# Performance work log

Hardware: AMD Instinct MI355X
Metric: run time of the kernel (lower is better)

The kernel has to match this reference:

```python
import jax, jax.numpy as jnp
import numpy as np

N_INST = 524288   # total instances across all bags
NF = 256          # feature dim
L = 128           # gated-attention hidden dim
C = 1             # num_classes
B = 4096          # num bags


def setup_inputs() -> dict:
    key = jax.random.key(0)
    k = jax.random.split(key, 6)
    # ragged bag sizes averaging ~128, deterministically summing to N_INST
    rng = np.random.RandomState(0)
    raw = rng.randint(64, 193, size=B).astype(np.int64)
    sizes = (raw * N_INST // raw.sum()).astype(np.int64)
    sizes[: int(N_INST - sizes.sum())] += 1  # distribute remainder (< B)
    assert sizes.sum() == N_INST
    s = 1.0 / np.sqrt(NF)
    return {
        "feats": jax.random.normal(k[0], (N_INST, NF), jnp.float32),
        "split_sizes": jnp.asarray(sizes, jnp.int64),
        "W_ins": jax.random.normal(k[1], (NF, C), jnp.float32) * s,
        "b_ins": jnp.zeros((C,), jnp.float32),
        "W_V": jax.random.normal(k[2], (NF, L), jnp.float32) * s,
        "b_V": jnp.zeros((L,), jnp.float32),
        "W_U": jax.random.normal(k[3], (NF, L), jnp.float32) * s,
        "b_U": jnp.zeros((L,), jnp.float32),
        "w_att": jax.random.normal(k[4], (L, 1), jnp.float32) * (1.0 / np.sqrt(L)),
        "b_att": jnp.zeros((1,), jnp.float32),
    }


def reference(feats, split_sizes, W_ins, b_ins, W_V, b_V, W_U, b_U, w_att, b_att):
    n = feats.shape[0]
    num_bags = split_sizes.shape[0]
    # segment id per instance (fused replacement of torch.split + Python loop)
    seg = jnp.repeat(jnp.arange(num_bags), split_sizes, total_repeat_length=n)

    # instance classifier (applied once to the whole ragged batch)
    inst_pred = feats @ W_ins + b_ins                      # [N, C]

    # gated attention scores
    gate = jnp.tanh(feats @ W_V + b_V) * jax.nn.sigmoid(feats @ W_U + b_U)
    scores = (gate @ w_att + b_att)[:, 0]                  # [N]

    # segmented softmax over each bag
    m = jax.ops.segment_max(scores, seg, num_segments=num_bags)  # [B]
    e = jnp.exp(scores - m[seg])
    denom = jax.ops.segment_sum(e, seg, num_segments=num_bags)   # [B]
    attn = e / denom[seg]                                        # [N]

    # bag prediction = attention-weighted sum of instance predictions
    bag_pred = jax.ops.segment_sum(attn[:, None] * inst_pred, seg,
                                   num_segments=num_bags)        # [B, C]
    return bag_pred, inst_pred
```

## Files before the change

### kernel.cpp

```cpp
#include <hip/hip_runtime.h>
#include <hip/hip_bf16.h>

#define N_INST 524288
#define NF     256
#define LDIM   128
#define NBAGS  4096
#define BM     64

typedef __attribute__((ext_vector_type(8)))  short          short8;
typedef __attribute__((ext_vector_type(16))) float          f32x16;
typedef __attribute__((ext_vector_type(4)))  unsigned short ushort4v;
typedef __attribute__((ext_vector_type(4)))  int            int4v;

__device__ __forceinline__ unsigned short f2bf(float f) {
    unsigned u = __float_as_uint(f);
    unsigned r = u + 0x7FFFu + ((u >> 16) & 1u);
    return (unsigned short)(r >> 16);
}

__global__ __launch_bounds__(256) void k_build(const float* __restrict__ W_V,
                                               const float* __restrict__ W_U,
                                               unsigned short* __restrict__ Bws) {
    int idx  = blockIdx.x * 256 + threadIdx.x;
    int j    = idx & 7;
    int lane = (idx >> 3) & 63;
    int ct   = (idx >> 9) & 7;
    int ks   = idx >> 12;
    int k    = ks * 16 + ((lane >> 5) << 3) + j;
    int n    = ((ct >> 1) << 5) + (lane & 31);
    const float* src = (ct & 1) ? W_U : W_V;
    Bws[idx] = f2bf(src[k * LDIM + n]);
}

__global__ __launch_bounds__(256) void k_scan(const int* __restrict__ sraw,
                                              int* __restrict__ offs) {
    __shared__ int csum[256];
    __shared__ int cpref[256];
    const int t = threadIdx.x;
    const bool is64 = (sraw[1] == 0);
    int local[16];
    int ssum = 0;
    for (int j = 0; j < 16; ++j) {
        int i = t * 16 + j;
        int v = is64 ? sraw[2 * i] : sraw[i];
        local[j] = v;
        ssum += v;
    }
    csum[t] = ssum;
    __syncthreads();
    if (t == 0) {
        int run = 0;
        for (int i = 0; i < 256; ++i) { cpref[i] = run; run += csum[i]; }
    }
    __syncthreads();
    int run = cpref[t];
    for (int j = 0; j < 16; ++j) { offs[t * 16 + j] = run; run += local[j]; }
    if (t == 255) offs[NBAGS] = run;
}

__global__ __launch_bounds__(256, 3) void k_gemm(
    const float* __restrict__ feats, const unsigned short* __restrict__ Bws,
    const float* __restrict__ W_ins, const float* __restrict__ b_ins,
    const float* __restrict__ b_V,   const float* __restrict__ b_U,
    const float* __restrict__ w_att, const float* __restrict__ b_att,
    float* __restrict__ scores, float* __restrict__ inst_out) {

    __shared__ unsigned short Al[2][1024];
    __shared__ float winsl[NF];
    __shared__ float bVl[LDIM], bUl[LDIM], wal[LDIM];
    __shared__ float Sp[BM][4];

    const int t    = threadIdx.x;
    const int lane = t & 63;
    const int cg   = t >> 6;
    const long r0  = (long)blockIdx.x * BM;

    const int row = t >> 2;
    const int q   = t & 3;

    winsl[t] = W_ins[t];
    if (t < LDIM) { bVl[t] = b_V[t]; bUl[t] = b_U[t]; wal[t] = w_att[t]; }

    const float*  arow = feats + (r0 + row) * NF + q * 4;
    const short8* bw   = (const short8*)Bws;

    const int aoff = ((row >> 5) * 64 + (q >> 1) * 32 + (row & 31)) * 8 + (q & 1) * 4;
    const int ctv  = cg * 2;
    const int ctu  = ctv + 1;

    float4 pa_0  = *(const float4*)(arow);
    short8 fbv_0 = bw[(0 * 8 + ctv) * 64 + lane];
    short8 fbu_0 = bw[(0 * 8 + ctu) * 64 + lane];
    float4 pa_1  = *(const float4*)(arow + 16);
    short8 fbv_1 = bw[(1 * 8 + ctv) * 64 + lane];
    short8 fbu_1 = bw[(1 * 8 + ctu) * 64 + lane];

    f32x16 accV0 = {}, accV1 = {};
    f32x16 accU0 = {}, accU1 = {};
    float pacc = 0.f;

    __syncthreads();

    #pragma unroll
    for (int ks = 0; ks < 16; ++ks) {
        const int X = ks & 1;
        float4 av  = X ? pa_1  : pa_0;
        short8 fbv = X ? fbv_1 : fbv_0;
        short8 fbu = X ? fbu_1 : fbu_0;

        float4 wv = *(const float4*)&winsl[ks * 16 + q * 4];
        pacc += av.x * wv.x + av.y * wv.y + av.z * wv.z + av.w * wv.w;

        ushort4v c;
        c.x = f2bf(av.x); c.y = f2bf(av.y); c.z = f2bf(av.z); c.w = f2bf(av.w);
        *(ushort4v*)&Al[X][aoff] = c;

        if (ks < 14) {
            if (X == 0) {
                pa_0  = *(const float4*)(arow + (ks + 2) * 16);
                fbv_0 = bw[((ks + 2) * 8 + ctv) * 64 + lane];
                fbu_0 = bw[((ks + 2) * 8 + ctu) * 64 + lane];
            } else {
                pa_1  = *(const float4*)(arow + (ks + 2) * 16);
                fbv_1 = bw[((ks + 2) * 8 + ctv) * 64 + lane];
                fbu_1 = bw[((ks + 2) * 8 + ctu) * 64 + lane];
            }
        }

        __syncthreads();

        short8 fa0 = *(const short8*)&Al[X][(0 * 64 + lane) * 8];
        short8 fa1 = *(const short8*)&Al[X][(1 * 64 + lane) * 8];
        accV0 = __builtin_amdgcn_mfma_f32_32x32x16_bf16(fa0, fbv, accV0, 0, 0, 0);
        accU0 = __builtin_amdgcn_mfma_f32_32x32x16_bf16(fa0, fbu, accU0, 0, 0, 0);
        accV1 = __builtin_amdgcn_mfma_f32_32x32x16_bf16(fa1, fbv, accV1, 0, 0, 0);
        accU1 = __builtin_amdgcn_mfma_f32_32x32x16_bf16(fa1, fbu, accU1, 0, 0, 0);
    }

    const int   c32 = lane & 31;
    const int   nn  = cg * 32 + c32;
    const float bv0s = bVl[nn], bu0s = bUl[nn], wn = wal[nn];
    const int   rh  = lane >> 5;

#define EPILOG(RT, AV, AU)                                                    \
    {                                                                         \
        _Pragma("unroll")                                                     \
        for (int r = 0; r < 16; ++r) {                                        \
            float v  = AV[r] + bv0s;                                          \
            float u  = AU[r] + bu0s;                                          \
            float ev = __expf(2.f * v);                                       \
            float th = 1.f - 2.f * __builtin_amdgcn_rcpf(ev + 1.f);           \
            float sg = __builtin_amdgcn_rcpf(1.f + __expf(-u));               \
            float x  = th * sg * wn;                                          \
            x += __shfl_xor(x, 1);                                            \
            x += __shfl_xor(x, 2);                                            \
            x += __shfl_xor(x, 4);                                            \
            x += __shfl_xor(x, 8);                                            \
            x += __shfl_xor(x, 16);                                           \
            if (c32 == 0)                                                     \
                Sp[RT * 32 + (r & 3) + 8 * (r >> 2) + 4 * rh][cg] = x;        \
        }                                                                     \
    }
    EPILOG(0, accV0, accU0)
    EPILOG(1, accV1, accU1)
#undef EPILOG

    float pt = pacc;
    pt += __shfl_xor(pt, 1);
    pt += __shfl_xor(pt, 2);
    if (q == 0) inst_out[r0 + row] = pt + b_ins[0];

    __syncthreads();
    if (t < BM)
        scores[r0 + t] = Sp[t][0] + Sp[t][1] + Sp[t][2] + Sp[t][3] + b_att[0];
}

__global__ __launch_bounds__(64) void k_bags(const int* __restrict__ offs,
                                             const float* __restrict__ scores,
                                             const float* __restrict__ inst,
                                             float* __restrict__ bag_out) {
    const int b    = blockIdx.x;
    const int lane = threadIdx.x;
    const int s0 = offs[b], s1 = offs[b + 1];
    float m = -1e30f;
    for (int i = s0 + lane; i < s1; i += 64) m = fmaxf(m, scores[i]);
    #pragma unroll
    for (int d = 32; d; d >>= 1) m = fmaxf(m, __shfl_xor(m, d));
    float se = 0.f, sp = 0.f;
    for (int i = s0 + lane; i < s1; i += 64) {
        float e = __expf(scores[i] - m);
        se += e;
        sp += e * inst[i];
    }
    #pragma unroll
    for (int d = 32; d; d >>= 1) { se += __shfl_xor(se, d); sp += __shfl_xor(sp, d); }
    if (lane == 0) bag_out[b] = sp / se;
}

extern "C" void kernel_launch(void* const* d_in, const int* in_sizes, int n_in,
                              void* d_out, int out_size, void* d_ws, size_t ws_size,
                              hipStream_t stream) {
    const float* feats  = (const float*)d_in[0];
    const int*   sizesr = (const int*)d_in[1];
    const float* W_ins  = (const float*)d_in[2];
    const float* b_ins  = (const float*)d_in[3];
    const float* W_V    = (const float*)d_in[4];
    const float* b_V    = (const float*)d_in[5];
    const float* W_U    = (const float*)d_in[6];
    const float* b_U    = (const float*)d_in[7];
    const float* w_att  = (const float*)d_in[8];
    const float* b_att  = (const float*)d_in[9];

    unsigned short* Bws    = (unsigned short*)d_ws;
    int*            offs   = (int*)((char*)d_ws + (128 << 10));
    float*          scores = (float*)((char*)d_ws + (160 << 10));

    float* bag_out  = (float*)d_out;
    float* inst_out = (float*)d_out + NBAGS;

    hipLaunchKernelGGL(k_build, dim3(256), dim3(256), 0, stream, W_V, W_U, Bws);
    hipLaunchKernelGGL(k_scan,  dim3(1),   dim3(256), 0, stream, sizesr, offs);
    hipLaunchKernelGGL(k_gemm,  dim3(N_INST / BM), dim3(256), 0, stream,
                       feats, Bws, W_ins, b_ins, b_V, b_U, w_att, b_att,
                       scores, inst_out);
    hipLaunchKernelGGL(k_bags,  dim3(NBAGS), dim3(64), 0, stream,
                       offs, scores, inst_out, bag_out);
}
```

Before: 898.1 us.

## Stage whole A tile in LDS up front and drop per-k-step barriers

Each thread now issues all 16 float4 loads of its feature row at once, converts them to bf16 and writes the full 64x256 A tile into a 32 KB LDS buffer, with a single barrier before the MFMA loop. This replaces the double-buffered two-stage pipeline that needed a __syncthreads every k-step. The W_ins dot product now reads directly from global memory instead of LDS. The cost is more LDS per block and higher register pressure from 16 live float4s, which may lower occupancy below the launch-bounds target and gives up overlap of A loads with MFMA work.

```diff
diff --git a/kernel.cpp b/kernel.cpp
--- a/kernel.cpp
+++ b/kernel.cpp
@@ -65,8 +65,7 @@
     const float* __restrict__ w_att, const float* __restrict__ b_att,
     float* __restrict__ scores, float* __restrict__ inst_out) {
 
-    __shared__ unsigned short Al[2][1024];
-    __shared__ float winsl[NF];
+    __shared__ unsigned short Al[16 * 1024];
     __shared__ float bVl[LDIM], bUl[LDIM], wal[LDIM];
     __shared__ float Sp[BM][4];
 
@@ -78,59 +77,66 @@
     const int row = t >> 2;
     const int q   = t & 3;
 
-    winsl[t] = W_ins[t];
-    if (t < LDIM) { bVl[t] = b_V[t]; bUl[t] = b_U[t]; wal[t] = w_att[t]; }
-
-    const float*  arow = feats + (r0 + row) * NF + q * 4;
-    const short8* bw   = (const short8*)Bws;
-
+    const float* arow = feats + (r0 + row) * NF + q * 4;
     const int aoff = ((row >> 5) * 64 + (q >> 1) * 32 + (row & 31)) * 8 + (q & 1) * 4;
-    const int ctv  = cg * 2;
-    const int ctu  = ctv + 1;
-
-    float4 pa_0  = *(const float4*)(arow);
+
+    float4 a0,a1,a2,a3,a4,a5,a6,a7,a8,a9,a10,a11,a12,a13,a14,a15;
+    a0  = *(const float4*)(arow +   0); a1  = *(const float4*)(arow +  16);
+    a2  = *(const float4*)(arow +  32); a3  = *(const float4*)(arow +  48);
+    a4  = *(const float4*)(arow +  64); a5  = *(const float4*)(arow +  80);
+    a6  = *(const float4*)(arow +  96); a7  = *(const float4*)(arow + 112);
+    a8  = *(const float4*)(arow + 128); a9  = *(const float4*)(arow + 144);
+    a10 = *(const float4*)(arow + 160); a11 = *(const float4*)(arow + 176);
+    a12 = *(const float4*)(arow + 192); a13 = *(const float4*)(arow + 208);
+    a14 = *(const float4*)(arow + 224); a15 = *(const float4*)(arow + 240);
+
+    const short8* bw  = (const short8*)Bws;
+    const int ctv = cg * 2;
+    const int ctu = ctv + 1;
     short8 fbv_0 = bw[(0 * 8 + ctv) * 64 + lane];
     short8 fbu_0 = bw[(0 * 8 + ctu) * 64 + lane];
-    float4 pa_1  = *(const float4*)(arow + 16);
     short8 fbv_1 = bw[(1 * 8 + ctv) * 64 + lane];
     short8 fbu_1 = bw[(1 * 8 + ctu) * 64 + lane];
 
+    if (t < LDIM) { bVl[t] = b_V[t]; bUl[t] = b_U[t]; wal[t] = w_att[t]; }
+
+    const float4* wq = (const float4*)W_ins + q;
+    float pacc = 0.f;
+#define STAGE(KS, AV)                                                         \
+    {                                                                         \
+        float4 wv = wq[(KS) * 4];                                             \
+        pacc += AV.x * wv.x + AV.y * wv.y + AV.z * wv.z + AV.w * wv.w;        \
+        ushort4v c;                                                           \
+        c.x = f2bf(AV.x); c.y = f2bf(AV.y); c.z = f2bf(AV.z); c.w = f2bf(AV.w);\
+        *(ushort4v*)&Al[(KS) * 1024 + aoff] = c;                              \
+    }
+    STAGE(0,  a0)  STAGE(1,  a1)  STAGE(2,  a2)  STAGE(3,  a3)
+    STAGE(4,  a4)  STAGE(5,  a5)  STAGE(6,  a6)  STAGE(7,  a7)
+    STAGE(8,  a8)  STAGE(9,  a9)  STAGE(10, a10) STAGE(11, a11)
+    STAGE(12, a12) STAGE(13, a13) STAGE(14, a14) STAGE(15, a15)
+#undef STAGE
+
     f32x16 accV0 = {}, accV1 = {};
     f32x16 accU0 = {}, accU1 = {};
-    float pacc = 0.f;
 
     __syncthreads();
 
     #pragma unroll
     for (int ks = 0; ks < 16; ++ks) {
         const int X = ks & 1;
-        float4 av  = X ? pa_1  : pa_0;
         short8 fbv = X ? fbv_1 : fbv_0;
         short8 fbu = X ? fbu_1 : fbu_0;
-
-        float4 wv = *(const float4*)&winsl[ks * 16 + q * 4];
-        pacc += av.x * wv.x + av.y * wv.y + av.z * wv.z + av.w * wv.w;
-
-        ushort4v c;
-        c.x = f2bf(av.x); c.y = f2bf(av.y); c.z = f2bf(av.z); c.w = f2bf(av.w);
-        *(ushort4v*)&Al[X][aoff] = c;
-
         if (ks < 14) {
             if (X == 0) {
-                pa_0  = *(const float4*)(arow + (ks + 2) * 16);
                 fbv_0 = bw[((ks + 2) * 8 + ctv) * 64 + lane];
                 fbu_0 = bw[((ks + 2) * 8 + ctu) * 64 + lane];
             } else {
-                pa_1  = *(const float4*)(arow + (ks + 2) * 16);
                 fbv_1 = bw[((ks + 2) * 8 + ctv) * 64 + lane];
                 fbu_1 = bw[((ks + 2) * 8 + ctu) * 64 + lane];
             }
         }
-
-        __syncthreads();
-
-        short8 fa0 = *(const short8*)&Al[X][(0 * 64 + lane) * 8];
-        short8 fa1 = *(const short8*)&Al[X][(1 * 64 + lane) * 8];
+        short8 fa0 = *(const short8*)&Al[ks * 1024 + (0 * 64 + lane) * 8];
+        short8 fa1 = *(const short8*)&Al[ks * 1024 + (1 * 64 + lane) * 8];
         accV0 = __builtin_amdgcn_mfma_f32_32x32x16_bf16(fa0, fbv, accV0, 0, 0, 0);
         accU0 = __builtin_amdgcn_mfma_f32_32x32x16_bf16(fa0, fbu, accU0, 0, 0, 0);
         accV1 = __builtin_amdgcn_mfma_f32_32x32x16_bf16(fa1, fbv, accV1, 0, 0, 0);
```

New measurement: 904.4 us. No clear change (+0.7%).
